# Optimization experiments

Hardware: AMD Instinct MI355X
Metric: run time of the kernel (lower is better)

Reference implementation:

```python
import jax, jax.numpy as jnp
import numpy as np

B, S_ENC, S_DEC, ENC_H, DEC_H = 8, 2048, 2048, 512, 512


def setup_inputs() -> dict:
    key = jax.random.key(0)
    k1, k2, k3 = jax.random.split(key, 3)
    return {
        "enc_hidden_states": jax.random.normal(k1, (B, S_ENC, ENC_H), dtype=jnp.float32),
        "dec_hidden_states": jax.random.normal(k2, (B, S_DEC, DEC_H), dtype=jnp.float32),
        "W_att": jax.random.normal(k3, (ENC_H, DEC_H), dtype=jnp.float32),
    }


def reference(enc_hidden_states, dec_hidden_states, W_att):
    # Project encoder states: [B, S_enc, dec_h]
    enc_proj = jnp.einsum("bse,ed->bsd", enc_hidden_states, W_att)
    # Luong 'general' scores for all decoder timesteps at once: [B, S_dec, S_enc]
    # (original code loops over decoder timesteps via tf.map_fn; this is the
    # equivalent single batched matmul)
    att_logits = jnp.einsum("btd,bsd->bts", dec_hidden_states, enc_proj)
    att_softmax = jax.nn.softmax(att_logits, axis=-1)
    # Attention context vectors: [B, S_dec, enc_h]
    att_vector = jnp.einsum("bts,bse->bte", att_softmax, enc_hidden_states)
    return att_vector
```

## Files before the change

kernel.cpp:

```cpp
#include <hip/hip_runtime.h>
#include <cstdint>


#define DEVINL __device__ __forceinline__

typedef __attribute__((ext_vector_type(8))) short short8;
typedef __attribute__((ext_vector_type(4))) float f32x4;

DEVINL short f2bf(float x) {
    union { float f; uint32_t u; } v; v.f = x;
    uint32_t r = v.u + 0x7FFFu + ((v.u >> 16) & 1u);
    return (short)(r >> 16);
}
DEVINL float bf2f(short h) {
    union { uint32_t u; float f; } v; v.u = ((uint32_t)(uint16_t)h) << 16;
    return v.f;
}

DEVINL void gload_lds16(const void* g, void* l) {
    __builtin_amdgcn_global_load_lds(
        (const __attribute__((address_space(1))) char*)g,
        (__attribute__((address_space(3))) char*)l, 16, 0, 0);
}

__global__ __launch_bounds__(256)
void split_kernel(const float* __restrict__ x, short* __restrict__ hi,
                  short* __restrict__ lo)
{
    long i = ((long)blockIdx.x * 256 + threadIdx.x) * 8;
    f32x4 a = *(const f32x4*)(x + i);
    f32x4 b = *(const f32x4*)(x + i + 4);
    short8 h, l;
#pragma unroll
    for (int j = 0; j < 4; j++) {
        short ha = f2bf(a[j]); h[j] = ha;     l[j] = f2bf(a[j] - bf2f(ha));
        short hb = f2bf(b[j]); h[4 + j] = hb; l[4 + j] = f2bf(b[j] - bf2f(hb));
    }
    *(short8*)(hi + i) = h;
    *(short8*)(lo + i) = l;
}

__global__ __launch_bounds__(256)
void split_w_kernel(const float* __restrict__ w, short* __restrict__ wth,
                    short* __restrict__ wtl)
{
    int idx = blockIdx.x * 256 + threadIdx.x;
    int k = idx >> 9, n = idx & 511;
    float v = w[idx];
    short h = f2bf(v);
    wth[(long)n * 512 + k] = h;
    wtl[(long)n * 512 + k] = f2bf(v - bf2f(h));
}

__global__ __launch_bounds__(256)
void transpose_bf16_kernel(const float* __restrict__ x, short* __restrict__ xt)
{
    __shared__ short tile[32][33];
    const int b  = blockIdx.z;
    const int s0 = blockIdx.x * 32;
    const int e0 = blockIdx.y * 32;
    const float* px = x + (long)b * 2048 * 512;
    short* pt = xt + (long)b * 512 * 2048;
    const int tx = threadIdx.x & 31;
    const int ty = threadIdx.x >> 5;
#pragma unroll
    for (int r = 0; r < 32; r += 8)
        tile[ty + r][tx] = f2bf(px[(long)(s0 + ty + r) * 512 + e0 + tx]);
    __syncthreads();
#pragma unroll
    for (int r = 0; r < 32; r += 8)
        pt[(long)(e0 + ty + r) * 2048 + s0 + tx] = tile[tx][ty + r];
}

template<int NTERMS, bool SPLIT_OUT>
__global__ __launch_bounds__(256, 2)
void gemm_bt(const short* __restrict__ Ah, const short* __restrict__ Al,
             const short* __restrict__ Bh, const short* __restrict__ Bl,
             float* __restrict__ C, short* __restrict__ Ch, short* __restrict__ Cl,
             int K, int lda, int ldb, int ldc,
             long sA, long sB, long sC)
{
    extern __shared__ char smem_raw[];
    constexpr int OPS = (NTERMS == 3) ? 4 : 2;
    constexpr int SET = 128 * 32 * OPS;
    short* smem = (short*)smem_raw;

    const int tid  = threadIdx.x;
    const int wave = tid >> 6;
    const int lane = tid & 63;
    const int quad = lane >> 4;
    const int l16  = lane & 15;
    const int wm   = (wave >> 1) * 64;
    const int wn   = (wave & 1) * 64;

    const long tile_m = (long)blockIdx.y * 128;
    const long tile_n = (long)blockIdx.x * 128;
    const int  bz     = blockIdx.z;

    const short* pAh = Ah + (long)bz * sA;
    const short* pBh = Bh + (long)bz * sB;
    const short* pAl = (NTERMS == 3) ? (Al + (long)bz * sA) : nullptr;
    const short* pBl = (NTERMS == 3) ? (Bl + (long)bz * sB) : nullptr;

    const int srow = tid >> 2;
    const int skq  = (tid & 3) * 8;
    const int lds_off = srow * 32 + skq;
    const long ga0 = (tile_m + srow) * (long)lda + skq;
    const long gb0 = (tile_n + srow) * (long)ldb + skq;

    auto stage = [&](int k0, int buf) {
        short* s   = smem + buf * SET;
        short* ash = s;
        short* bsh = s + 128 * 32;
        gload_lds16(pAh + ga0 + k0,             ash + lds_off);
        gload_lds16(pAh + ga0 + 64l * lda + k0, ash + lds_off + 64 * 32);
        gload_lds16(pBh + gb0 + k0,             bsh + lds_off);
        gload_lds16(pBh + gb0 + 64l * ldb + k0, bsh + lds_off + 64 * 32);
        if constexpr (NTERMS == 3) {
            short* asl = s + 2 * 128 * 32;
            short* bsl = s + 3 * 128 * 32;
            gload_lds16(pAl + ga0 + k0,             asl + lds_off);
            gload_lds16(pAl + ga0 + 64l * lda + k0, asl + lds_off + 64 * 32);
            gload_lds16(pBl + gb0 + k0,             bsl + lds_off);
            gload_lds16(pBl + gb0 + 64l * ldb + k0, bsl + lds_off + 64 * 32);
        }
    };

    f32x4 acc[4][4] = {};
    stage(0, 0);
    int cur = 0;

    for (int k0 = 0; k0 < K; k0 += 32) {
        __syncthreads();
        if (k0 + 32 < K) stage(k0 + 32, cur ^ 1);

        short* s   = smem + cur * SET;
        short* ash = s;
        short* bsh = s + 128 * 32;
        short* asl = s + 2 * 128 * 32;
        short* bsl = s + 3 * 128 * 32;

        short8 ah[4], bh[4], al[4], bl[4];
#pragma unroll
        for (int i = 0; i < 4; i++) {
            ah[i] = *(const short8*)&ash[(wm + i * 16 + l16) * 32 + quad * 8];
            bh[i] = *(const short8*)&bsh[(wn + i * 16 + l16) * 32 + quad * 8];
            if constexpr (NTERMS == 3) {
                al[i] = *(const short8*)&asl[(wm + i * 16 + l16) * 32 + quad * 8];
                bl[i] = *(const short8*)&bsl[(wn + i * 16 + l16) * 32 + quad * 8];
            }
        }
#pragma unroll
        for (int i = 0; i < 4; i++)
#pragma unroll
            for (int j = 0; j < 4; j++) {
                acc[i][j] = __builtin_amdgcn_mfma_f32_16x16x32_bf16(ah[i], bh[j], acc[i][j], 0, 0, 0);
                if constexpr (NTERMS == 3) {
                    acc[i][j] = __builtin_amdgcn_mfma_f32_16x16x32_bf16(ah[i], bl[j], acc[i][j], 0, 0, 0);
                    acc[i][j] = __builtin_amdgcn_mfma_f32_16x16x32_bf16(al[i], bh[j], acc[i][j], 0, 0, 0);
                }
            }
        cur ^= 1;
    }

#pragma unroll
    for (int i = 0; i < 4; i++)
#pragma unroll
        for (int j = 0; j < 4; j++) {
            const long row0 = tile_m + wm + i * 16 + quad * 4;
            const long col  = tile_n + wn + j * 16 + l16;
#pragma unroll
            for (int r = 0; r < 4; r++) {
                float v = acc[i][j][r];
                if constexpr (SPLIT_OUT) {
                    long idx = (long)bz * sC + (row0 + r) * (long)ldc + col;
                    short h = f2bf(v);
                    Ch[idx] = h;
                    Cl[idx] = f2bf(v - bf2f(h));
                } else {
                    C[(long)bz * sC + (row0 + r) * (long)ldc + col] = v;
                }
            }
        }
}

__global__ __launch_bounds__(256)
void softmax_kernel(const float* __restrict__ logits, short* __restrict__ P)
{
    const long row = blockIdx.x;
    const float* p = logits + row * 2048;
    const int tid = threadIdx.x;
    const int lane = tid & 63, wave = tid >> 6;

    f32x4 v0 = *(const f32x4*)(p + tid * 8);
    f32x4 v1 = *(const f32x4*)(p + tid * 8 + 4);

    float m = fmaxf(fmaxf(fmaxf(v0[0], v0[1]), fmaxf(v0[2], v0[3])),
                    fmaxf(fmaxf(v1[0], v1[1]), fmaxf(v1[2], v1[3])));
#pragma unroll
    for (int o = 32; o > 0; o >>= 1) m = fmaxf(m, __shfl_xor(m, o));

    __shared__ float red[8];
    if (lane == 0) red[wave] = m;
    __syncthreads();
    m = fmaxf(fmaxf(red[0], red[1]), fmaxf(red[2], red[3]));

    float e[8];
    float s = 0.f;
#pragma unroll
    for (int i = 0; i < 4; i++) { e[i] = __expf(v0[i] - m); s += e[i]; }
#pragma unroll
    for (int i = 0; i < 4; i++) { e[4 + i] = __expf(v1[i] - m); s += e[4 + i]; }
#pragma unroll
    for (int o = 32; o > 0; o >>= 1) s += __shfl_xor(s, o);
    if (lane == 0) red[4 + wave] = s;
    __syncthreads();
    const float inv = 1.f / (red[4] + red[5] + red[6] + red[7]);

    short8 ob;
#pragma unroll
    for (int i = 0; i < 8; i++) ob[i] = f2bf(e[i] * inv);
    *(short8*)(P + row * 2048 + tid * 8) = ob;
}

extern "C" void kernel_launch(void* const* d_in, const int* in_sizes, int n_in,
                              void* d_out, int out_size, void* d_ws, size_t ws_size,
                              hipStream_t stream)
{
    const float* enc = (const float*)d_in[0];
    const float* dec = (const float*)d_in[1];
    const float* W   = (const float*)d_in[2];
    float* out = (float*)d_out;

    const long BSE = 8l * 2048 * 512;
    const long NW  = 512l * 512;

    char* p = (char*)d_ws;
    auto take = [&](long bytes) { char* r = p; p += (bytes + 255) & ~255l; return r; };
    short* enc_hi = (short*)take(BSE * 2);
    short* enc_lo = (short*)take(BSE * 2);
    short* dec_hi = (short*)take(BSE * 2);
    short* dec_lo = (short*)take(BSE * 2);
    short* ep_hi  = (short*)take(BSE * 2);
    short* ep_lo  = (short*)take(BSE * 2);
    short* enc_t  = (short*)take(BSE * 2);
    short* wt_hi  = (short*)take(NW * 2);
    short* wt_lo  = (short*)take(NW * 2);
    float* logits = (float*)take(8l * 2048 * 2048 * 4);
    short* Pbuf = enc_hi;
    (void)ws_size; (void)in_sizes; (void)n_in; (void)out_size;

    split_kernel<<<4096, 256, 0, stream>>>(enc, enc_hi, enc_lo);
    split_kernel<<<4096, 256, 0, stream>>>(dec, dec_hi, dec_lo);
    split_w_kernel<<<1024, 256, 0, stream>>>(W, wt_hi, wt_lo);
    transpose_bf16_kernel<<<dim3(64, 16, 8), 256, 0, stream>>>(enc, enc_t);

    gemm_bt<3, true><<<dim3(4, 128, 1), 256, 64 * 1024, stream>>>(
        enc_hi, enc_lo, wt_hi, wt_lo, nullptr, ep_hi, ep_lo,
        512, 512, 512, 512, 0, 0, 0);

    gemm_bt<3, false><<<dim3(16, 16, 8), 256, 64 * 1024, stream>>>(
        dec_hi, dec_lo, ep_hi, ep_lo, logits, nullptr, nullptr,
        512, 512, 512, 2048, 2048l * 512, 2048l * 512, 2048l * 2048);

    softmax_kernel<<<16384, 256, 0, stream>>>(logits, Pbuf);

    gemm_bt<1, false><<<dim3(4, 16, 8), 256, 32 * 1024, stream>>>(
        Pbuf, nullptr, enc_t, nullptr, out, nullptr, nullptr,
        2048, 2048, 2048, 512, 2048l * 2048, 512l * 2048, 2048l * 512);
}
```

Measured before the change: 357.9 us.

## Add 256x256-tile split-bf16 GEMM kernel for attention logits

```diff
diff --git a/kernel.cpp b/kernel.cpp
--- a/kernel.cpp
+++ b/kernel.cpp
@@ -184,6 +184,132 @@
         }
 }
 
+__global__ __launch_bounds__(512, 2)
+void gemm3_256(const short* __restrict__ Ah, const short* __restrict__ Al,
+               const short* __restrict__ Bh, const short* __restrict__ Bl,
+               float* __restrict__ C,
+               int K, int lda, int ldb, int ldc,
+               long sA, long sB, long sC, int nbx, int nby)
+{
+    extern __shared__ char smem_raw[];
+    short* smem = (short*)smem_raw;
+    constexpr int PL  = 256 * 32;
+    constexpr int SET = 4 * PL;
+
+    const int t    = threadIdx.x;
+    const int wave = t >> 6;
+    const int lane = t & 63;
+    const int quad = lane >> 4;
+    const int l16  = lane & 15;
+    const int wm   = (wave >> 2) * 128;
+    const int wn   = (wave & 3) * 64;
+    const int kslot8 = ((quad ^ ((l16 >> 1) & 3)) << 3);
+
+    const int nwg = gridDim.x;
+    const int wg  = blockIdx.x;
+    const int swz = (wg & 7) * (nwg >> 3) + (wg >> 3);
+    const int per_b = nbx * nby;
+    const int bz  = swz / per_b;
+    const int rem = swz - bz * per_b;
+    const long tile_m = (long)(rem / nbx) * 256;
+    const long tile_n = (long)(rem % nbx) * 256;
+
+    const short* pAh = Ah + (long)bz * sA;
+    const short* pAl = Al + (long)bz * sA;
+    const short* pBh = Bh + (long)bz * sB;
+    const short* pBl = Bl + (long)bz * sB;
+
+    const int srow   = t >> 2;
+    const int schunk = (t & 3) ^ ((t >> 3) & 3);
+    const long gA  = (tile_m + srow) * (long)lda + schunk * 8;
+    const long gB  = (tile_n + srow) * (long)ldb + schunk * 8;
+    const long gA2 = gA + 128l * lda;
+    const long gB2 = gB + 128l * ldb;
+    const int ld0 = t * 8;
+
+    auto stage = [&](int k0, int buf) {
+        short* s = smem + buf * SET;
+        gload_lds16(pAh + gA  + k0, s + ld0);
+        gload_lds16(pAh + gA2 + k0, s + ld0 + 4096);
+        gload_lds16(pAl + gA  + k0, s + PL + ld0);
+        gload_lds16(pAl + gA2 + k0, s + PL + ld0 + 4096);
+        gload_lds16(pBh + gB  + k0, s + 2 * PL + ld0);
+        gload_lds16(pBh + gB2 + k0, s + 2 * PL + ld0 + 4096);
+        gload_lds16(pBl + gB  + k0, s + 3 * PL + ld0);
+        gload_lds16(pBl + gB2 + k0, s + 3 * PL + ld0 + 4096);
+    };
+
+    f32x4 acc[8][4] = {};
+    stage(0, 0);
+    int cur = 0;
+
+    for (int k0 = 0; k0 < K; k0 += 32) {
+        if (k0 + 32 < K) {
+            stage(k0 + 32, cur ^ 1);
+            asm volatile("s_waitcnt vmcnt(8)" ::: "memory");
+        } else {
+            asm volatile("s_waitcnt vmcnt(0)" ::: "memory");
+        }
+        __builtin_amdgcn_s_barrier();
+
+        const short* s    = smem + cur * SET;
+        const short* ah_p = s;
+        const short* al_p = s + PL;
+        const short* bh_p = s + 2 * PL;
+        const short* bl_p = s + 3 * PL;
+
+        short8 bh[4], bl[4], ah[4], al[4];
+#pragma unroll
+        for (int j = 0; j < 4; j++) {
+            bh[j] = *(const short8*)&bh_p[(wn + j * 16 + l16) * 32 + kslot8];
+            bl[j] = *(const short8*)&bl_p[(wn + j * 16 + l16) * 32 + kslot8];
+        }
+#pragma unroll
+        for (int i = 0; i < 4; i++) {
+            ah[i] = *(const short8*)&ah_p[(wm + i * 16 + l16) * 32 + kslot8];
+            al[i] = *(const short8*)&al_p[(wm + i * 16 + l16) * 32 + kslot8];
+        }
+        __builtin_amdgcn_s_setprio(1);
+#pragma unroll
+        for (int i = 0; i < 4; i++)
+#pragma unroll
+            for (int j = 0; j < 4; j++) {
+                acc[i][j] = __builtin_amdgcn_mfma_f32_16x16x32_bf16(ah[i], bh[j], acc[i][j], 0, 0, 0);
+                acc[i][j] = __builtin_amdgcn_mfma_f32_16x16x32_bf16(ah[i], bl[j], acc[i][j], 0, 0, 0);
+                acc[i][j] = __builtin_amdgcn_mfma_f32_16x16x32_bf16(al[i], bh[j], acc[i][j], 0, 0, 0);
+            }
+        __builtin_amdgcn_s_setprio(0);
+#pragma unroll
+        for (int i = 0; i < 4; i++) {
+            ah[i] = *(const short8*)&ah_p[(wm + 64 + i * 16 + l16) * 32 + kslot8];
+            al[i] = *(const short8*)&al_p[(wm + 64 + i * 16 + l16) * 32 + kslot8];
+        }
+        __builtin_amdgcn_s_setprio(1);
+#pragma unroll
+        for (int i = 0; i < 4; i++)
+#pragma unroll
+            for (int j = 0; j < 4; j++) {
+                acc[4 + i][j] = __builtin_amdgcn_mfma_f32_16x16x32_bf16(ah[i], bh[j], acc[4 + i][j], 0, 0, 0);
+                acc[4 + i][j] = __builtin_amdgcn_mfma_f32_16x16x32_bf16(ah[i], bl[j], acc[4 + i][j], 0, 0, 0);
+                acc[4 + i][j] = __builtin_amdgcn_mfma_f32_16x16x32_bf16(al[i], bh[j], acc[4 + i][j], 0, 0, 0);
+            }
+        __builtin_amdgcn_s_setprio(0);
+        __builtin_amdgcn_s_barrier();
+        cur ^= 1;
+    }
+
+#pragma unroll
+    for (int i = 0; i < 8; i++)
+#pragma unroll
+        for (int j = 0; j < 4; j++) {
+            const long row0 = tile_m + wm + i * 16 + quad * 4;
+            const long col  = tile_n + wn + j * 16 + l16;
+#pragma unroll
+            for (int r = 0; r < 4; r++)
+                C[(long)bz * sC + (row0 + r) * (long)ldc + col] = acc[i][j][r];
+        }
+}
+
 __global__ __launch_bounds__(256)
 void softmax_kernel(const float* __restrict__ logits, short* __restrict__ P)
 {
@@ -250,6 +376,14 @@
     short* Pbuf = enc_hi;
     (void)ws_size; (void)in_sizes; (void)n_in; (void)out_size;
 
+    static bool attr_set = false;
+    if (!attr_set) {
+        (void)hipFuncSetAttribute((const void*)gemm3_256,
+                                  hipFuncAttributeMaxDynamicSharedMemorySize,
+                                  131072);
+        attr_set = true;
+    }
+
     split_kernel<<<4096, 256, 0, stream>>>(enc, enc_hi, enc_lo);
     split_kernel<<<4096, 256, 0, stream>>>(dec, dec_hi, dec_lo);
     split_w_kernel<<<1024, 256, 0, stream>>>(W, wt_hi, wt_lo);
@@ -259,9 +393,9 @@
         enc_hi, enc_lo, wt_hi, wt_lo, nullptr, ep_hi, ep_lo,
         512, 512, 512, 512, 0, 0, 0);
 
-    gemm_bt<3, false><<<dim3(16, 16, 8), 256, 64 * 1024, stream>>>(
-        dec_hi, dec_lo, ep_hi, ep_lo, logits, nullptr, nullptr,
-        512, 512, 512, 2048, 2048l * 512, 2048l * 512, 2048l * 2048);
+    gemm3_256<<<512, 512, 131072, stream>>>(
+        dec_hi, dec_lo, ep_hi, ep_lo, logits,
+        512, 512, 512, 2048, 2048l * 512, 2048l * 512, 2048l * 2048, 8, 8);
 
     softmax_kernel<<<16384, 256, 0, stream>>>(logits, Pbuf);
 
```

Result: faster. 350.0 us (-2.2%).
